# Kernel tuning notes

Measured on AMD Instinct MI355X. Metric: run time of the kernel, lower is better.

The kernel has to match this reference:

```python
import jax, jax.numpy as jnp
import numpy as np

B, S, D, H, DH = 4, 2048, 512, 8, 64

def setup_inputs() -> dict:
    key = jax.random.key(0)
    k1, k2, k3, k4 = jax.random.split(key, 4)
    sc = 1.0 / np.sqrt(D)
    return {
        "x": jax.random.normal(k1, (B, S, D), dtype=jnp.float32),
        "Wq": jax.random.normal(k2, (H, D, DH), dtype=jnp.float32) * sc,
        "Wk": jax.random.normal(k3, (H, D, DH), dtype=jnp.float32) * sc,
        "Wv": jax.random.normal(k4, (H, D, DH), dtype=jnp.float32) * sc,
    }

def reference(x, Wq, Wk, Wv):
    # x: [B,S,D]; Wq/Wk/Wv: [H,D,DH] (stacked per-head bias-free Linear weights)
    q = jnp.einsum('bsd,hdk->bhsk', x, Wq)
    k = jnp.einsum('bsd,hdk->bhsk', x, Wk)
    v = jnp.einsum('bsd,hdk->bhsk', x, Wv)
    scale = DH ** -0.5
    scores = jax.nn.softmax(jnp.einsum('bhqk,bhsk->bhqs', q, k) * scale, axis=-1)
    out = jnp.einsum('bhqs,bhsk->bhqk', scores, v)  # [B,H,S,DH]
    # concat heads along last dim (head order matches ModuleList order)
    return out.transpose(0, 2, 1, 3).reshape(B, S, H * DH)
```

## Files before the change

kernel.cpp:

```cpp
#include <hip/hip_runtime.h>

typedef _Float16 half8  __attribute__((ext_vector_type(8)));
typedef _Float16 half4v __attribute__((ext_vector_type(4)));
typedef _Float16 half2v __attribute__((ext_vector_type(2)));
typedef __fp16   fp16x2 __attribute__((ext_vector_type(2)));
typedef float    float4v __attribute__((ext_vector_type(4)));

#define CSC 0.18033688f

__device__ __forceinline__ void async16(const _Float16* g, void* l) {
    __builtin_amdgcn_global_load_lds((const __attribute__((address_space(1))) void*)g,
                                     (__attribute__((address_space(3))) void*)l, 16, 0, 0);
}

__device__ __forceinline__ half2v pk2(float a, float b) {
    return __builtin_bit_cast(half2v, __builtin_amdgcn_cvt_pkrtz(a, b));
}

__global__ __launch_bounds__(256) void mha_prep(const float* __restrict__ x,
    const float* __restrict__ wq, const float* __restrict__ wk, const float* __restrict__ wv,
    _Float16* __restrict__ xh, _Float16* __restrict__ wt) {
    __shared__ __align__(16) _Float16 T[64][72];
    const int tid = threadIdx.x;
    if (blockIdx.x < 4096) {
        int t = blockIdx.x * 256 + tid;
        float4v v = ((const float4v*)x)[t];
        half4v o;
        #pragma unroll
        for (int i = 0; i < 4; ++i) o[i] = (_Float16)v[i];
        ((half4v*)xh)[t] = o;
        return;
    }
    const int blk = blockIdx.x - 4096;
    const int dt = blk & 7, h = (blk >> 3) & 7, mat = blk >> 6;
    const float* w = ((mat == 0) ? wq : (mat == 1) ? wk : wv) + h * 32768 + dt * 64 * 64;
    #pragma unroll
    for (int i = 0; i < 4; ++i) {
        int s = tid + i * 256;
        int dl = s >> 4, c4 = s & 15;
        float4v v = ((const float4v*)(w + (size_t)dl * 64))[c4];
        #pragma unroll
        for (int e = 0; e < 4; ++e) T[c4 * 4 + e][dl] = (_Float16)v[e];
    }
    __syncthreads();
    #pragma unroll
    for (int i = 0; i < 2; ++i) {
        int s = tid + i * 256;
        int dh = s >> 3, c8 = s & 7;
        half8 o;
        #pragma unroll
        for (int e = 0; e < 8; ++e) o[e] = T[dh][c8 * 8 + e];
        *(half8*)(wt + (size_t)((mat * 8 + h) * 64 + dh) * 512 + dt * 64 + c8 * 8) = o;
    }
}

__global__ __launch_bounds__(256, 3) void mha_qkv(const _Float16* __restrict__ xh,
    const _Float16* __restrict__ wt, _Float16* __restrict__ Qm, _Float16* __restrict__ Km,
    _Float16* __restrict__ Vt) {
    __shared__ __align__(16) char smem[34816];
    _Float16* Ash[2] = { (_Float16*)smem,           (_Float16*)(smem + 8192)  };
    _Float16* Bsh[2] = { (_Float16*)(smem + 16384), (_Float16*)(smem + 24576) };
    const int tid = threadIdx.x;
    const int lane = tid & 63, wave = tid >> 6;
    const int quad = lane >> 4, li = lane & 15;
    const int m0 = blockIdx.x * 128, n0 = blockIdx.y * 128;
    float4v acc[4][4] = {};
    const int r0 = tid >> 2, c0 = (tid & 3) ^ ((r0 >> 1) & 3);
    const int s1 = 256 + tid, r1 = s1 >> 2, c1 = (s1 & 3) ^ ((r1 >> 1) & 3);
    const _Float16* gA0 = xh + (size_t)(m0 + r0) * 512 + c0 * 8;
    const _Float16* gA1 = xh + (size_t)(m0 + r1) * 512 + c1 * 8;
    const _Float16* gB0 = wt + (size_t)(n0 + r0) * 512 + c0 * 8;
    const _Float16* gB1 = wt + (size_t)(n0 + r1) * 512 + c1 * 8;
    const int wr = (wave >> 1) * 64, wc = (wave & 1) * 64;
    const char* aB[2]; const char* bB[2];
    #pragma unroll
    for (int bb = 0; bb < 2; ++bb) {
        aB[bb] = (const char*)Ash[bb] + (wr + li) * 64 + ((quad ^ ((li >> 1) & 3)) << 4);
        bB[bb] = (const char*)Bsh[bb] + (wc + li) * 64 + ((quad ^ ((li >> 1) & 3)) << 4);
    }
    auto stage = [&](int bb, int kk) {
        async16(gA0 + kk, (char*)Ash[bb] + wave * 1024);
        async16(gA1 + kk, (char*)Ash[bb] + 4096 + wave * 1024);
        async16(gB0 + kk, (char*)Bsh[bb] + wave * 1024);
        async16(gB1 + kk, (char*)Bsh[bb] + 4096 + wave * 1024);
    };
    auto compute = [&](int bb) {
        half8 af[4], bf[4];
        #pragma unroll
        for (int mt = 0; mt < 4; ++mt) af[mt] = *(const half8*)(aB[bb] + mt * 1024);
        #pragma unroll
        for (int nt = 0; nt < 4; ++nt) bf[nt] = *(const half8*)(bB[bb] + nt * 1024);
        #pragma unroll
        for (int mt = 0; mt < 4; ++mt)
            #pragma unroll
            for (int nt = 0; nt < 4; ++nt)
                acc[mt][nt] = __builtin_amdgcn_mfma_f32_16x16x32_f16(af[mt], bf[nt], acc[mt][nt], 0, 0, 0);
    };
    stage(0, 0);
    for (int kk = 0; kk < 512; kk += 64) {
        __syncthreads();
        stage(1, kk + 32);
        compute(0);
        __syncthreads();
        if (kk + 64 < 512) stage(0, kk + 64);
        compute(1);
    }
    const int mat = n0 >> 9;
    if (mat == 2) {
        #pragma unroll
        for (int mt = 0; mt < 4; ++mt) {
            int m = m0 + wr + mt * 16 + quad * 4;
            int b = m >> 11, s = m & 2047;
            #pragma unroll
            for (int nt = 0; nt < 4; ++nt) {
                int n = n0 + wc + nt * 16 + li;
                int h = (n >> 6) & 7, dh = n & 63;
                int bh = b * 8 + h;
                half4v pkv;
                #pragma unroll
                for (int r = 0; r < 4; ++r) pkv[r] = (_Float16)acc[mt][nt][r];
                *(half4v*)(Vt + ((size_t)bh * 64 + dh) * 2048 + s) = pkv;
            }
        }
    } else {
        _Float16* dst = (mat == 0) ? Qm : Km;
        const float osc = (mat == 0) ? CSC : 1.0f;
        __syncthreads();
        char* Tb = smem;
        #pragma unroll
        for (int mt = 0; mt < 4; ++mt) {
            int rbase = wr + mt * 16 + quad * 4;
            #pragma unroll
            for (int nt = 0; nt < 4; ++nt) {
                int col = wc + nt * 16 + li;
                #pragma unroll
                for (int r = 0; r < 4; ++r)
                    *(_Float16*)(Tb + (rbase + r) * 272 + col * 2) = (_Float16)(acc[mt][nt][r] * osc);
            }
        }
        __syncthreads();
        const int h0 = (n0 >> 6) & 7;
        #pragma unroll
        for (int i = 0; i < 8; ++i) {
            int c = i * 256 + tid;
            int row = c >> 4, j8 = c & 15;
            half8 v = *(const half8*)(Tb + row * 272 + j8 * 16);
            int m = m0 + row;
            int b = m >> 11, s = m & 2047;
            int bh = b * 8 + h0 + (j8 >> 3);
            *(half8*)(dst + ((size_t)bh * 2048 + s) * 64 + (j8 & 7) * 8) = v;
        }
    }
}

__global__ __launch_bounds__(256, 2) void mha_attn(const _Float16* __restrict__ Qm,
    const _Float16* __restrict__ Km, const _Float16* __restrict__ Vt, float* __restrict__ out) {
    __shared__ __align__(16) _Float16 KtA[4][64 * 64];
    __shared__ __align__(16) _Float16 VtA[4][64 * 64];
    const int tid = threadIdx.x, lane = tid & 63, wave = tid >> 6;
    const int quad = lane >> 4, li = lane & 15;
    const int strm = wave & 1, hh = wave >> 1;
    const int flat = blockIdx.x;
    const int qb = (flat >> 3) & 15;
    const int bh = ((flat >> 7) << 3) | (flat & 7);
    const int b = bh >> 3, h = bh & 7;
    const _Float16* Qg = Qm + (size_t)bh * 2048 * 64;
    const _Float16* Kg = Km + (size_t)bh * 2048 * 64 + (size_t)strm * 1024 * 64;
    const _Float16* Vg = Vt + (size_t)bh * 64 * 2048 + (size_t)strm * 1024;
    const int q0 = qb * 128 + hh * 64;
    half8 qf[4][2];
    #pragma unroll
    for (int qt = 0; qt < 4; ++qt)
        #pragma unroll
        for (int ds = 0; ds < 2; ++ds)
            qf[qt][ds] = *(const half8*)(Qg + (size_t)(q0 + qt * 16 + li) * 64 + ds * 32 + quad * 8);
    half8 vone;
    #pragma unroll
    for (int e = 0; e < 8; ++e) vone[e] = (_Float16)1.0f;
    float4v O[4][4] = {};
    float4v O4[4] = {};
    char* Kst[2]; char* Vst[2];
    #pragma unroll
    for (int bb = 0; bb < 2; ++bb) {
        Kst[bb] = (char*)KtA + (strm * 2 + bb) * 8192;
        Vst[bb] = (char*)VtA + (strm * 2 + bb) * 8192;
    }
    const _Float16* pK[4]; const _Float16* pV[4];
    #pragma unroll
    for (int is = 0; is < 4; ++is) {
        int c = is * 128 + hh * 64 + lane;
        int rk = c >> 3, sck = c & 7;
        int swk = (rk & 3) | (((rk >> 3) & 1) << 2);
        int rv = c >> 3, cv = (c & 7) ^ (rv & 7);
        pK[is] = Kg + (size_t)rk * 64 + (sck ^ swk) * 8;
        pV[is] = Vg + (size_t)rv * 2048 + cv * 8;
    }
    auto stage = [&](int bb) {
        #pragma unroll
        for (int is = 0; is < 4; ++is) {
            async16(pK[is], Kst[bb] + is * 2048 + hh * 1024);
            async16(pV[is], Vst[bb] + is * 2048 + hh * 1024);
            pK[is] += 4096;
            pV[is] += 64;
        }
    };
    const int rowE = ((li >> 2) << 3) | (li & 3);
    const int swzE = (li & 3) | (((li >> 2) & 1) << 2);
    const char *k0e[2], *k1e[2], *vBq[2];
    #pragma unroll
    for (int bb = 0; bb < 2; ++bb) {
        k0e[bb] = Kst[bb] + rowE * 128 + ((quad ^ swzE) << 4);
        k1e[bb] = Kst[bb] + rowE * 128 + (((quad + 4) ^ swzE) << 4);
        vBq[bb] = Vst[bb] + li * 128;
    }
    int coff[2];
    #pragma unroll
    for (int c = 0; c < 2; ++c) coff[c] = (((c * 4 + quad) ^ (li & 7)) << 4);
    auto compute = [&](int bb) {
        #pragma unroll
        for (int c = 0; c < 2; ++c) {
            half8 f0e = *(const half8*)(k0e[bb] + c * 4096);
            half8 f1e = *(const half8*)(k1e[bb] + c * 4096);
            half8 f0o = *(const half8*)(k0e[bb] + c * 4096 + 512);
            half8 f1o = *(const half8*)(k1e[bb] + c * 4096 + 512);
            half8 pf[4];
            #pragma unroll
            for (int qt = 0; qt < 4; ++qt) {
                float4v se = {}, so = {};
                __builtin_amdgcn_s_setprio(1);
                se = __builtin_amdgcn_mfma_f32_16x16x32_f16(f0e, qf[qt][0], se, 0, 0, 0);
                se = __builtin_amdgcn_mfma_f32_16x16x32_f16(f1e, qf[qt][1], se, 0, 0, 0);
                so = __builtin_amdgcn_mfma_f32_16x16x32_f16(f0o, qf[qt][0], so, 0, 0, 0);
                so = __builtin_amdgcn_mfma_f32_16x16x32_f16(f1o, qf[qt][1], so, 0, 0, 0);
                __builtin_amdgcn_s_setprio(0);
                float pe[4], po[4];
                #pragma unroll
                for (int r = 0; r < 4; ++r) {
                    pe[r] = __builtin_amdgcn_exp2f(se[r]);
                    po[r] = __builtin_amdgcn_exp2f(so[r]);
                }
                half4v a = __builtin_shufflevector(pk2(pe[0], pe[1]), pk2(pe[2], pe[3]), 0, 1, 2, 3);
                half4v o = __builtin_shufflevector(pk2(po[0], po[1]), pk2(po[2], po[3]), 0, 1, 2, 3);
                pf[qt] = __builtin_shufflevector(a, o, 0, 1, 2, 3, 4, 5, 6, 7);
            }
            __builtin_amdgcn_s_setprio(1);
            #pragma unroll
            for (int qt = 0; qt < 4; ++qt)
                O4[qt] = __builtin_amdgcn_mfma_f32_16x16x32_f16(pf[qt], vone, O4[qt], 0, 0, 0);
            #pragma unroll
            for (int dt = 0; dt < 4; ++dt) {
                half8 vf = *(const half8*)(vBq[bb] + dt * 2048 + coff[c]);
                #pragma unroll
                for (int qt = 0; qt < 4; ++qt)
                    O[qt][dt] = __builtin_amdgcn_mfma_f32_16x16x32_f16(pf[qt], vf, O[qt][dt], 0, 0, 0);
            }
            __builtin_amdgcn_s_setprio(0);
        }
    };
    stage(0);
    for (int it = 0; it < 8; ++it) {
        __syncthreads();
        stage(1);
        compute(0);
        __syncthreads();
        if (it < 7) stage(0);
        compute(1);
    }
    __syncthreads();
    float* Obuf = (float*)KtA;
    float* Lbuf = (float*)VtA;
    if (strm == 1) {
        #pragma unroll
        for (int qt = 0; qt < 4; ++qt) {
            #pragma unroll
            for (int dt = 0; dt < 4; ++dt)
                ((float4v*)(Obuf + hh * 4096))[(qt * 4 + dt) * 64 + lane] = O[qt][dt];
            ((float4v*)(Lbuf + hh * 1024))[qt * 64 + lane] = O4[qt];
        }
    }
    __syncthreads();
    if (strm == 1) return;
    #pragma unroll
    for (int qt = 0; qt < 4; ++qt) {
        #pragma unroll
        for (int dt = 0; dt < 4; ++dt) {
            float4v o2 = ((float4v*)(Obuf + hh * 4096))[(qt * 4 + dt) * 64 + lane];
            O[qt][dt] += o2;
        }
        float4v l2 = ((float4v*)(Lbuf + hh * 1024))[qt * 64 + lane];
        O4[qt] += l2;
    }
    #pragma unroll
    for (int qt = 0; qt < 4; ++qt) {
        #pragma unroll
        for (int r = 0; r < 4; ++r) {
            float inv = 1.0f / O4[qt][r];
            int q = q0 + qt * 16 + quad * 4 + r;
            float* orow = out + ((size_t)(b * 2048 + q)) * 512 + h * 64;
            #pragma unroll
            for (int dt = 0; dt < 4; ++dt) orow[dt * 16 + li] = O[qt][dt][r] * inv;
        }
    }
}

extern "C" void kernel_launch(void* const* d_in, const int* in_sizes, int n_in,
                              void* d_out, int out_size, void* d_ws, size_t ws_size,
                              hipStream_t stream) {
    const float* x  = (const float*)d_in[0];
    const float* wq = (const float*)d_in[1];
    const float* wk = (const float*)d_in[2];
    const float* wv = (const float*)d_in[3];
    float* out = (float*)d_out;
    char* ws = (char*)d_ws;
    _Float16* xh = (_Float16*)(ws);
    _Float16* wt = (_Float16*)(ws + 8388608);
    _Float16* Qm = (_Float16*)(ws + 9961472);
    _Float16* Km = (_Float16*)(ws + 18350080);
    _Float16* Vt = (_Float16*)(ws + 26738688);
    if (ws_size < 35127296u) return;
    mha_prep<<<4288, 256, 0, stream>>>(x, wq, wk, wv, xh, wt);
    mha_qkv<<<dim3(64, 12), 256, 0, stream>>>(xh, wt, Qm, Km, Vt);
    mha_attn<<<512, 256, 0, stream>>>(Qm, Km, Vt, out);
}
```

Before: 132.1 us.

## Load K/V fragments directly from global memory and remap blocks per XCD

Removes the LDS double-buffered async staging of K and V tiles and the barriers around it. Each wave now loads its MFMA K and V fragments straight from global memory, relying on L2 and cache reuse across waves. The block index mapping is also changed so that all query blocks of a given batch-head land on the same XCD, which should improve L2 locality. The cost is more redundant global and L2 traffic and no explicit overlap of loads with compute.

```diff
diff --git a/kernel.cpp b/kernel.cpp
--- a/kernel.cpp
+++ b/kernel.cpp
@@ -155,14 +155,14 @@
 
 __global__ __launch_bounds__(256, 2) void mha_attn(const _Float16* __restrict__ Qm,
     const _Float16* __restrict__ Km, const _Float16* __restrict__ Vt, float* __restrict__ out) {
-    __shared__ __align__(16) _Float16 KtA[4][64 * 64];
-    __shared__ __align__(16) _Float16 VtA[4][64 * 64];
+    __shared__ __align__(16) char mrg[40960];
     const int tid = threadIdx.x, lane = tid & 63, wave = tid >> 6;
     const int quad = lane >> 4, li = lane & 15;
     const int strm = wave & 1, hh = wave >> 1;
     const int flat = blockIdx.x;
-    const int qb = (flat >> 3) & 15;
-    const int bh = ((flat >> 7) << 3) | (flat & 7);
+    const int xcd = flat & 7, n = flat >> 3;
+    const int bh = xcd * 4 + (n & 3);
+    const int qb = n >> 2;
     const int b = bh >> 3, h = bh & 7;
     const _Float16* Qg = Qm + (size_t)bh * 2048 * 64;
     const _Float16* Kg = Km + (size_t)bh * 2048 * 64 + (size_t)strm * 1024 * 64;
@@ -179,50 +179,19 @@
     for (int e = 0; e < 8; ++e) vone[e] = (_Float16)1.0f;
     float4v O[4][4] = {};
     float4v O4[4] = {};
-    char* Kst[2]; char* Vst[2];
-    #pragma unroll
-    for (int bb = 0; bb < 2; ++bb) {
-        Kst[bb] = (char*)KtA + (strm * 2 + bb) * 8192;
-        Vst[bb] = (char*)VtA + (strm * 2 + bb) * 8192;
-    }
-    const _Float16* pK[4]; const _Float16* pV[4];
-    #pragma unroll
-    for (int is = 0; is < 4; ++is) {
-        int c = is * 128 + hh * 64 + lane;
-        int rk = c >> 3, sck = c & 7;
-        int swk = (rk & 3) | (((rk >> 3) & 1) << 2);
-        int rv = c >> 3, cv = (c & 7) ^ (rv & 7);
-        pK[is] = Kg + (size_t)rk * 64 + (sck ^ swk) * 8;
-        pV[is] = Vg + (size_t)rv * 2048 + cv * 8;
-    }
-    auto stage = [&](int bb) {
-        #pragma unroll
-        for (int is = 0; is < 4; ++is) {
-            async16(pK[is], Kst[bb] + is * 2048 + hh * 1024);
-            async16(pV[is], Vst[bb] + is * 2048 + hh * 1024);
-            pK[is] += 4096;
-            pV[is] += 64;
-        }
-    };
-    const int rowE = ((li >> 2) << 3) | (li & 3);
-    const int swzE = (li & 3) | (((li >> 2) & 1) << 2);
-    const char *k0e[2], *k1e[2], *vBq[2];
-    #pragma unroll
-    for (int bb = 0; bb < 2; ++bb) {
-        k0e[bb] = Kst[bb] + rowE * 128 + ((quad ^ swzE) << 4);
-        k1e[bb] = Kst[bb] + rowE * 128 + (((quad + 4) ^ swzE) << 4);
-        vBq[bb] = Vst[bb] + li * 128;
-    }
-    int coff[2];
-    #pragma unroll
-    for (int c = 0; c < 2; ++c) coff[c] = (((c * 4 + quad) ^ (li & 7)) << 4);
-    auto compute = [&](int bb) {
+    const int rE = ((li >> 2) << 3) | (li & 3);
+    const _Float16* kRow = Kg + (size_t)rE * 64 + quad * 8;
+    const _Float16* vRow = Vg + (size_t)li * 2048 + quad * 8;
+    #pragma unroll 2
+    for (int t = 0; t < 16; ++t) {
+        const int kb = t * 64;
         #pragma unroll
         for (int c = 0; c < 2; ++c) {
-            half8 f0e = *(const half8*)(k0e[bb] + c * 4096);
-            half8 f1e = *(const half8*)(k1e[bb] + c * 4096);
-            half8 f0o = *(const half8*)(k0e[bb] + c * 4096 + 512);
-            half8 f1o = *(const half8*)(k1e[bb] + c * 4096 + 512);
+            const _Float16* kc = kRow + (size_t)(kb + c * 32) * 64;
+            half8 f0e = *(const half8*)(kc);
+            half8 f1e = *(const half8*)(kc + 32);
+            half8 f0o = *(const half8*)(kc + 256);
+            half8 f1o = *(const half8*)(kc + 288);
             half8 pf[4];
             #pragma unroll
             for (int qt = 0; qt < 4; ++qt) {
@@ -249,26 +218,17 @@
                 O4[qt] = __builtin_amdgcn_mfma_f32_16x16x32_f16(pf[qt], vone, O4[qt], 0, 0, 0);
             #pragma unroll
             for (int dt = 0; dt < 4; ++dt) {
-                half8 vf = *(const half8*)(vBq[bb] + dt * 2048 + coff[c]);
+                half8 vf = *(const half8*)(vRow + (size_t)dt * 32768 + kb + c * 32);
                 #pragma unroll
                 for (int qt = 0; qt < 4; ++qt)
                     O[qt][dt] = __builtin_amdgcn_mfma_f32_16x16x32_f16(pf[qt], vf, O[qt][dt], 0, 0, 0);
             }
             __builtin_amdgcn_s_setprio(0);
         }
-    };
-    stage(0);
-    for (int it = 0; it < 8; ++it) {
-        __syncthreads();
-        stage(1);
-        compute(0);
-        __syncthreads();
-        if (it < 7) stage(0);
-        compute(1);
     }
     __syncthreads();
-    float* Obuf = (float*)KtA;
-    float* Lbuf = (float*)VtA;
+    float* Obuf = (float*)mrg;
+    float* Lbuf = (float*)(mrg + 32768);
     if (strm == 1) {
         #pragma unroll
         for (int qt = 0; qt < 4; ++qt) {
```

Measured after the change: 156.9 us. +18.8%, slower.
